# Kernel optimization log

Hardware: AMD Instinct MI355X
Metric: run time of the kernel (lower is better)

Reference implementation:

```python
import jax, jax.numpy as jnp
import numpy as np
import math

KERNEL_SIZES = [3, 5, 7, 7, 9, 9]
DILATIONS = [1, 2, 1, 3, 1, 2]
NUM_HEADS = 6
HEAD_DIM = 32  # in_channels 192 / 6 heads


def _neighborhood_patches(t, k, dil):
    """Equivalent of F.unfold(t, kernel_size=k, dilation=dil, padding=dil*(k//2)).
    t: [B, d, H, W] -> [B, d, k*k, H, W] (zero-padded borders, torch unfold ordering:
    patch index p = i*k + j over the kernel window, row-major)."""
    B, d, H, W = t.shape
    pad = dil * (k // 2)
    tp = jnp.pad(t, ((0, 0), (0, 0), (pad, pad), (pad, pad)))
    pats = [tp[:, :, i * dil:i * dil + H, j * dil:j * dil + W]
            for i in range(k) for j in range(k)]
    return jnp.stack(pats, axis=2)


def setup_inputs() -> dict:
    key = jax.random.key(0)
    ks = jax.random.split(key, 3 + NUM_HEADS)
    B, C, H, W = 4, 192, 96, 96
    x = jax.random.normal(ks[0], (B, C, H, W), dtype=jnp.float32)
    w_qkv = jax.random.normal(ks[1], (3 * C, C), dtype=jnp.float32) * 0.02  # 1x1 conv weight
    w_out = jax.random.normal(ks[2], (C, C), dtype=jnp.float32) * 0.02      # 1x1 conv weight
    inp = {"x": x, "w_qkv": w_qkv, "w_out": w_out}
    for i, k in enumerate(KERNEL_SIZES):
        # module inits biases to zeros; use small randn so softmax path is exercised
        inp[f"b{i}"] = jax.random.normal(ks[3 + i], (k * k,), dtype=jnp.float32) * 0.02
    return inp


def reference(x, w_qkv, w_out, b0, b1, b2, b3, b4, b5):
    biases = [b0, b1, b2, b3, b4, b5]
    B, C, H, W = x.shape
    scale = 1.0 / math.sqrt(HEAD_DIM)
    # 1x1 conv qkv projection
    qkv = jnp.einsum('bchw,oc->bohw', x, w_qkv)
    q, k, v = jnp.split(qkv, 3, axis=1)
    q = q.reshape(B, NUM_HEADS, HEAD_DIM, H, W)
    k = k.reshape(B, NUM_HEADS, HEAD_DIM, H, W)
    v = v.reshape(B, NUM_HEADS, HEAD_DIM, H, W)
    head_outs = []
    for i in range(NUM_HEADS):  # heads have structurally different (k, dilation)
        ksz, dil = KERNEL_SIZES[i], DILATIONS[i]
        kp = _neighborhood_patches(k[:, i], ksz, dil)  # [B, d, k*k, H, W]
        vp = _neighborhood_patches(v[:, i], ksz, dil)  # [B, d, k*k, H, W]
        scores = jnp.einsum('bdhw,bdphw->bphw', q[:, i], kp) * scale
        scores = scores + biases[i][None, :, None, None]
        attn = jax.nn.softmax(scores, axis=1)  # softmax over the k*k neighborhood
        head_outs.append(jnp.einsum('bphw,bdphw->bdhw', attn, vp))
    out = jnp.concatenate(head_outs, axis=1)  # [B, C, H, W]
    return jnp.einsum('bchw,oc->bohw', out, w_out)
```

## Files before the change

kernel.cpp:

```cpp
#include <hip/hip_runtime.h>
#include <hip/hip_bf16.h>
#include <math.h>

#define NPIX 9216
#define HDIM 96
#define WDIM 96
#define NHEADS 6
#define BATCH 4

typedef __bf16 bf16x8 __attribute__((ext_vector_type(8)));
typedef float  f32x4  __attribute__((ext_vector_type(4)));

struct Bias6 { const float* p[6]; };

__device__ __forceinline__ void cp16(void* ldst, const void* gsrc) {
    __builtin_amdgcn_global_load_lds(
        (const __attribute__((address_space(1))) unsigned int*)gsrc,
        (__attribute__((address_space(3))) unsigned int*)ldst, 16, 0, 0);
}

__device__ __forceinline__ unsigned short bfbits(__bf16 x) { return *(unsigned short*)&x; }

__device__ __forceinline__ unsigned packf16(float a, float b) {
    _Float16 ha = (_Float16)a, hb = (_Float16)b;
    return (unsigned)*(unsigned short*)&ha | ((unsigned)*(unsigned short*)&hb << 16);
}

template<int N>
__device__ __forceinline__ void waitcnt_vm() {
    if constexpr (N == 0) asm volatile("s_waitcnt vmcnt(0)" ::: "memory");
    else if constexpr (N == 2) asm volatile("s_waitcnt vmcnt(2)" ::: "memory");
    else if constexpr (N == 3) asm volatile("s_waitcnt vmcnt(3)" ::: "memory");
    else if constexpr (N == 5) asm volatile("s_waitcnt vmcnt(5)" ::: "memory");
    else asm volatile("s_waitcnt vmcnt(0)" ::: "memory");
    __builtin_amdgcn_sched_barrier(0);
}

#define MIX_LL(acc, kk, qq) asm("v_fma_mix_f32 %0, %1, %2, %0 op_sel:[0,0,0] op_sel_hi:[1,1,0]" : "+v"(acc) : "v"(kk), "v"(qq))
#define MIX_HH(acc, kk, qq) asm("v_fma_mix_f32 %0, %1, %2, %0 op_sel:[1,1,0] op_sel_hi:[1,1,0]" : "+v"(acc) : "v"(kk), "v"(qq))
#define MIX_LF(acc, vv, ee) asm("v_fma_mix_f32 %0, %1, %2, %0 op_sel:[0,0,0] op_sel_hi:[1,0,0]" : "+v"(acc) : "v"(vv), "v"(ee))
#define MIX_HF(acc, vv, ee) asm("v_fma_mix_f32 %0, %1, %2, %0 op_sel:[1,0,0] op_sel_hi:[1,0,0]" : "+v"(acc) : "v"(vv), "v"(ee))

__global__ __launch_bounds__(256) void convert_x(
    const float* __restrict__ x, __bf16* __restrict__ Xh,
    const float* __restrict__ w1, __bf16* __restrict__ h1, __bf16* __restrict__ l1,
    const float* __restrict__ w2, __bf16* __restrict__ h2, __bf16* __restrict__ l2)
{
    __shared__ float t[32][65];
    const int b  = blockIdx.z;
    const int c0 = blockIdx.y * 32;
    const int p0 = blockIdx.x * 64;
    const int tid = threadIdx.x;

    if (blockIdx.y == 0 && blockIdx.z == 0) {
        const int f = blockIdx.x * 256 + tid;
        #pragma unroll
        for (int u = 0; u < 4; ++u) {
            const int i = f * 4 + u;
            if (i < 576 * 192) {
                float v = w1[i]; __bf16 h = (__bf16)v;
                h1[i] = h; l1[i] = (__bf16)(v - (float)h);
            } else {
                const int j = i - 576 * 192;
                float v = w2[j]; __bf16 h = (__bf16)v;
                h2[j] = h; l2[j] = (__bf16)(v - (float)h);
            }
        }
    }

    const int pl = tid & 63;
    #pragma unroll
    for (int i = 0; i < 8; ++i) {
        const int c = i * 4 + (tid >> 6);
        t[c][pl] = x[((size_t)b * 192 + c0 + c) * NPIX + p0 + pl];
    }
    __syncthreads();
    const int p  = tid >> 2;
    const int cq = (tid & 3) * 8;
    bf16x8 vh;
    #pragma unroll
    for (int j = 0; j < 8; ++j)
        vh[j] = (__bf16)t[cq + j][p];
    *(bf16x8*)(Xh + ((size_t)b * NPIX + p0 + p) * 192 + c0 + cq) = vh;
}

template<int MODE, int TWO_FROM>
__global__ __launch_bounds__(256) void gemm_mfma(
    const __bf16* __restrict__ Ah, const __bf16* __restrict__ Al,
    const __bf16* __restrict__ Bh,
    void* __restrict__ Yv, int M)
{
    __shared__ __bf16 sAh[64 * 64];
    __shared__ __bf16 sAl[64 * 64];
    __shared__ __bf16 sBh[128 * 64];

    const int b  = blockIdx.z;
    const int n0 = blockIdx.x * 128;
    const int m0 = blockIdx.y * 64;
    const bool two = (TWO_FROM < 1024) && (m0 >= TWO_FROM);
    const int tid  = threadIdx.x;
    const int lane = tid & 63;
    const int wid  = tid >> 6;
    const int wr = wid >> 1, wc = wid & 1;
    const int lr = lane & 15;
    const int kg = lane >> 4;

    const char* gA_h = (const char*)Ah + (size_t)m0 * 384;
    const char* gA_l = (const char*)Al + (size_t)m0 * 384;
    const char* gB   = (const char*)Bh + ((size_t)b * NPIX + n0) * 384;

    f32x4 acc[2][4];
    #pragma unroll
    for (int mf = 0; mf < 2; ++mf)
        #pragma unroll
        for (int nf = 0; nf < 4; ++nf)
            acc[mf][nf] = (f32x4){0.f, 0.f, 0.f, 0.f};

    for (int ks = 0; ks < 3; ++ks) {
        if (ks) __syncthreads();
        const int kb = ks * 128;
        #pragma unroll
        for (int it = 0; it < 2; ++it) {
            const int d  = it * 256 + tid;
            const int rd = d >> 3, cd = d & 7;
            const size_t src = (size_t)rd * 384 + kb + ((cd ^ (rd & 7)) << 4);
            cp16((char*)sAh + d * 16, gA_h + src);
            if (two) cp16((char*)sAl + d * 16, gA_l + src);
        }
        #pragma unroll
        for (int it = 0; it < 4; ++it) {
            const int d  = it * 256 + tid;
            const int rd = d >> 3, cd = d & 7;
            const size_t src = (size_t)rd * 384 + kb + ((cd ^ (rd & 7)) << 4);
            cp16((char*)sBh + d * 16, gB + src);
        }
        __syncthreads();
        #pragma unroll
        for (int s = 0; s < 2; ++s) {
            bf16x8 aH[2], aL[2], bH[4];
            #pragma unroll
            for (int mf = 0; mf < 2; ++mf) {
                const int row = wr * 32 + mf * 16 + lr;
                const int c = (s * 4 + kg) ^ (row & 7);
                aH[mf] = *(const bf16x8*)((const char*)sAh + row * 128 + c * 16);
                if (two) aL[mf] = *(const bf16x8*)((const char*)sAl + row * 128 + c * 16);
            }
            #pragma unroll
            for (int nf = 0; nf < 4; ++nf) {
                const int row = wc * 64 + nf * 16 + lr;
                const int c = (s * 4 + kg) ^ (row & 7);
                bH[nf] = *(const bf16x8*)((const char*)sBh + row * 128 + c * 16);
            }
            #pragma unroll
            for (int mf = 0; mf < 2; ++mf)
                #pragma unroll
                for (int nf = 0; nf < 4; ++nf) {
                    acc[mf][nf] = __builtin_amdgcn_mfma_f32_16x16x32_bf16(aH[mf], bH[nf], acc[mf][nf], 0, 0, 0);
                    if (two)
                        acc[mf][nf] = __builtin_amdgcn_mfma_f32_16x16x32_bf16(aL[mf], bH[nf], acc[mf][nf], 0, 0, 0);
                }
        }
    }

    if (MODE == 0) {
        float* Yb = (float*)Yv + ((size_t)b * M + m0 + wr * 32) * NPIX + n0 + wc * 64;
        #pragma unroll
        for (int mf = 0; mf < 2; ++mf)
            #pragma unroll
            for (int r = 0; r < 4; ++r) {
                const int row = mf * 16 + kg * 4 + r;
                #pragma unroll
                for (int nf = 0; nf < 4; ++nf)
                    Yb[(size_t)row * NPIX + nf * 16 + lr] = acc[mf][nf][r];
            }
    } else {
        #pragma unroll
        for (int mf = 0; mf < 2; ++mf) {
            const int cbase = m0 + wr * 32 + mf * 16 + kg * 4;
            unsigned* Yq = (unsigned*)Yv
                + (((size_t)b * 72 + (cbase >> 3)) * NPIX + n0 + wc * 64 + lr) * 4
                + ((kg & 1) << 1);
            #pragma unroll
            for (int nf = 0; nf < 4; ++nf) {
                Yq[(nf * 16) * 4 + 0] = packf16(acc[mf][nf][0], acc[mf][nf][1]);
                Yq[(nf * 16) * 4 + 1] = packf16(acc[mf][nf][2], acc[mf][nf][3]);
            }
        }
    }
}

template<int KSZ, int DIL, bool DB, int L>
__device__ __forceinline__ void attn_body(
    const uint4* __restrict__ Qq, const uint4* __restrict__ Kq,
    const uint4* __restrict__ Vq, const float* __restrict__ bias,
    const uint4* __restrict__ guard,
    __bf16* __restrict__ oh, int h0, int w0,
    uint4* __restrict__ bufs,
    unsigned (* __restrict__ out_lds)[256])
{
    constexpr int CC  = KSZ / 2;
    constexpr int HAL = CC * DIL;
    constexpr int R   = 8 + 2 * HAL;
    constexpr int C   = 32 + 2 * HAL;
    constexpr int RC  = R * C;
    constexpr int NN  = KSZ * KSZ;

    const int tid = threadIdx.x;
    const int tx = tid & 31;
    const int ty = tid >> 5;
    const int pix = (h0 + ty) * WDIM + (w0 + tx);
    const int lb = ty * C + tx;

    uint4 qv[4];
    #pragma unroll
    for (int p = 0; p < 4; ++p) qv[p] = Qq[(size_t)p * NPIX + pix];

    float score[NN];
    #pragma unroll
    for (int n = 0; n < NN; ++n) score[n] = bias[n] * 5.656854249492381f;

    auto STAGE = [&](int r) {
        const uint4* src = (r < 4) ? (Kq + (size_t)r * NPIX)
                                   : (Vq + (size_t)(r - 4) * NPIX);
        uint4* dst = bufs + (DB ? ((r & 1) * (L * 256)) : 0);
        #pragma unroll
        for (int it = 0; it < L; ++it) {
            const int idx = it * 256 + tid;
            const int rr = idx / C, cc = idx - rr * C;
            const int gh = h0 - HAL + rr, gw = w0 - HAL + cc;
            const bool ok = (idx < RC) && ((unsigned)gh < (unsigned)HDIM)
                                       && ((unsigned)gw < (unsigned)WDIM);
            const uint4* s = ok ? (src + gh * WDIM + gw) : guard;
            cp16(dst + idx, s);
        }
    };

    auto QK = [&](const uint4* buf, int oct) {
        const uint4 q = qv[oct];
        #pragma unroll
        for (int i = 0; i < KSZ; ++i)
            #pragma unroll
            for (int j = 0; j < KSZ; ++j) {
                const uint4 k8 = buf[lb + i * DIL * C + j * DIL];
                float s = score[i * KSZ + j];
                MIX_LL(s, k8.x, q.x); MIX_HH(s, k8.x, q.x);
                MIX_LL(s, k8.y, q.y); MIX_HH(s, k8.y, q.y);
                MIX_LL(s, k8.z, q.z); MIX_HH(s, k8.z, q.z);
                MIX_LL(s, k8.w, q.w); MIX_HH(s, k8.w, q.w);
                score[i * KSZ + j] = s;
            }
    };

    float inv = 0.f;
    auto SOFTMAX = [&]() {
        float l = 0.f;
        #pragma unroll
        for (int n = 0; n < NN; ++n) {
            const float e = exp2f(score[n] * 0.25506113952980654f);
            l += e;
            score[n] = e;
        }
        inv = 1.f / l;
    };

    auto PV = [&](const uint4* buf, int oct) {
        float a0 = 0.f, a1 = 0.f, a2 = 0.f, a3 = 0.f;
        float a4 = 0.f, a5 = 0.f, a6 = 0.f, a7 = 0.f;
        #pragma unroll
        for (int i = 0; i < KSZ; ++i)
            #pragma unroll
            for (int j = 0; j < KSZ; ++j) {
                const uint4 v8 = buf[lb + i * DIL * C + j * DIL];
                const float e = score[i * KSZ + j];
                MIX_LF(a0, v8.x, e); MIX_HF(a1, v8.x, e);
                MIX_LF(a2, v8.y, e); MIX_HF(a3, v8.y, e);
                MIX_LF(a4, v8.z, e); MIX_HF(a5, v8.z, e);
                MIX_LF(a6, v8.w, e); MIX_HF(a7, v8.w, e);
            }
        const int rr = oct & 1;
        const __bf16 c0 = (__bf16)(a0 * inv), c1 = (__bf16)(a1 * inv);
        const __bf16 c2 = (__bf16)(a2 * inv), c3 = (__bf16)(a3 * inv);
        const __bf16 c4 = (__bf16)(a4 * inv), c5 = (__bf16)(a5 * inv);
        const __bf16 c6 = (__bf16)(a6 * inv), c7 = (__bf16)(a7 * inv);
        out_lds[rr * 4 + 0][tid] = (unsigned)bfbits(c0) | ((unsigned)bfbits(c1) << 16);
        out_lds[rr * 4 + 1][tid] = (unsigned)bfbits(c2) | ((unsigned)bfbits(c3) << 16);
        out_lds[rr * 4 + 2][tid] = (unsigned)bfbits(c4) | ((unsigned)bfbits(c5) << 16);
        out_lds[rr * 4 + 3][tid] = (unsigned)bfbits(c6) | ((unsigned)bfbits(c7) << 16);
    };

    auto COOP = [&](int half) {
        #pragma unroll
        for (int it = 0; it < 2; ++it) {
            const int linear = it * 256 + tid;
            const int px = linear >> 1;
            const int c  = linear & 1;
            const int gpix = (h0 + (px >> 5)) * WDIM + w0 + (px & 31);
            uint4 val = make_uint4(out_lds[c * 4 + 0][px], out_lds[c * 4 + 1][px],
                                   out_lds[c * 4 + 2][px], out_lds[c * 4 + 3][px]);
            *((uint4*)((unsigned*)(oh + (size_t)gpix * 192)) + half * 2 + c) = val;
        }
    };

    if constexpr (DB) {
        STAGE(0);
        #pragma unroll
        for (int r = 0; r < 8; ++r) {
            if (r < 7) STAGE(r + 1);
            if (r < 7) waitcnt_vm<L>(); else waitcnt_vm<0>();
            __builtin_amdgcn_s_barrier();
            __builtin_amdgcn_sched_barrier(0);
            const uint4* buf = bufs + (r & 1) * (L * 256);
            if (r < 4) {
                QK(buf, r);
                if (r == 3) SOFTMAX();
            } else {
                PV(buf, r - 4);
                asm volatile("s_waitcnt lgkmcnt(0)" ::: "memory");
                __builtin_amdgcn_sched_barrier(0);
            }
            __builtin_amdgcn_s_barrier();
            __builtin_amdgcn_sched_barrier(0);
            if (r == 5) COOP(0);
            if (r == 7) COOP(1);
        }
    } else {
        #pragma unroll
        for (int r = 0; r < 8; ++r) {
            __syncthreads();
            if (r == 6) COOP(0);
            STAGE(r);
            __syncthreads();
            const uint4* buf = bufs;
            if (r < 4) {
                QK(buf, r);
                if (r == 3) SOFTMAX();
            } else {
                PV(buf, r - 4);
            }
        }
        __syncthreads();
        COOP(1);
    }
}

__global__ __launch_bounds__(256) void attn_kernel(
    const uint4* __restrict__ qkv, Bias6 bs, __bf16* __restrict__ ATh,
    const uint4* __restrict__ guard)
{
    __shared__ uint4 bufs[2560];
    __shared__ unsigned out_lds[8][256];

    const int orig = blockIdx.x;
    const int wg = (orig & 7) * 108 + (orig >> 3);
    const int panel = wg / 36;
    const int tile = wg - panel * 36;
    const int chunk = panel / 3, slot = panel - chunk * 3;
    int head, b;
    if (slot == 0)      { head = 4 + (chunk >> 2); b = chunk & 3; }
    else if (slot == 1) { head = 2 + (chunk >> 2); b = chunk & 3; }
    else                { head = (chunk < 4) ? 1 : 0; b = chunk & 3; }
    const int tx = tile % 3, ty = tile / 3;
    const int w0 = tx * 32, h0 = ty * 8;

    const uint4* base = qkv + (size_t)b * 72 * NPIX;
    const uint4* Qq = base + (size_t)(head * 4) * NPIX;
    const uint4* Kq = base + (size_t)(24 + head * 4) * NPIX;
    const uint4* Vq = base + (size_t)(48 + head * 4) * NPIX;
    __bf16* oh = ATh + (size_t)b * NPIX * 192 + head * 32;
    const float* bias = bs.p[head];

    switch (head) {
        case 0: attn_body<3, 1, true, 2>(Qq, Kq, Vq, bias, guard, oh, h0, w0, bufs, out_lds); break;
        case 1: attn_body<5, 2, true, 3>(Qq, Kq, Vq, bias, guard, oh, h0, w0, bufs, out_lds); break;
        case 2: attn_body<7, 1, true, 3>(Qq, Kq, Vq, bias, guard, oh, h0, w0, bufs, out_lds); break;
        case 3: attn_body<7, 3, false, 6>(Qq, Kq, Vq, bias, guard, oh, h0, w0, bufs, out_lds); break;
        case 4: attn_body<9, 1, true, 3>(Qq, Kq, Vq, bias, guard, oh, h0, w0, bufs, out_lds); break;
        case 5: attn_body<9, 2, true, 5>(Qq, Kq, Vq, bias, guard, oh, h0, w0, bufs, out_lds); break;
    }
}

extern "C" void kernel_launch(void* const* d_in, const int* in_sizes, int n_in,
                              void* d_out, int out_size, void* d_ws, size_t ws_size,
                              hipStream_t stream) {
    const float* x     = (const float*)d_in[0];
    const float* w_qkv = (const float*)d_in[1];
    const float* w_out = (const float*)d_in[2];
    Bias6 bs;
    for (int i = 0; i < 6; ++i) bs.p[i] = (const float*)d_in[3 + i];
    float* out = (float*)d_out;

    char* ws = (char*)d_ws;
    uint4* QKV = (uint4*)ws;            ws += (size_t)BATCH * 72 * NPIX * 16;
    __bf16* Xh  = (__bf16*)ws;          ws += (size_t)BATCH * NPIX * 192 * 2;
    __bf16* ATh = (__bf16*)ws;          ws += (size_t)BATCH * NPIX * 192 * 2;
    __bf16* W1h = (__bf16*)ws;          ws += (size_t)576 * 192 * 2;
    __bf16* W1l = (__bf16*)ws;          ws += (size_t)576 * 192 * 2;
    __bf16* W2h = (__bf16*)ws;          ws += (size_t)192 * 192 * 2;
    __bf16* W2l = (__bf16*)ws;          ws += (size_t)192 * 192 * 2;
    uint4* guard = (uint4*)ws;          ws += 1024;

    hipMemsetAsync(guard, 0, 1024, stream);

    convert_x<<<dim3(NPIX / 64, 192 / 32, BATCH), 256, 0, stream>>>(
        x, Xh, w_qkv, W1h, W1l, w_out, W2h, W2l);

    gemm_mfma<1, 384><<<dim3(NPIX / 128, 576 / 64, BATCH), 256, 0, stream>>>(
        W1h, W1l, Xh, (void*)QKV, 576);

    attn_kernel<<<dim3(864), 256, 0, stream>>>(QKV, bs, ATh, guard);

    gemm_mfma<0, 1024><<<dim3(NPIX / 128, 192 / 64, BATCH), 256, 0, stream>>>(
        W2h, W2l, ATh, (void*)out, 192);
}
```

Baseline: 91.35 us.

## Switch GEMMs to fp16 single-pass MFMA and remap grid across XCDs

```diff
diff --git a/kernel.cpp b/kernel.cpp
--- a/kernel.cpp
+++ b/kernel.cpp
@@ -8,8 +8,8 @@
 #define NHEADS 6
 #define BATCH 4
 
-typedef __bf16 bf16x8 __attribute__((ext_vector_type(8)));
-typedef float  f32x4  __attribute__((ext_vector_type(4)));
+typedef _Float16 f16x8 __attribute__((ext_vector_type(8)));
+typedef float    f32x4 __attribute__((ext_vector_type(4)));
 
 struct Bias6 { const float* p[6]; };
 
@@ -18,8 +18,6 @@
         (const __attribute__((address_space(1))) unsigned int*)gsrc,
         (__attribute__((address_space(3))) unsigned int*)ldst, 16, 0, 0);
 }
-
-__device__ __forceinline__ unsigned short bfbits(__bf16 x) { return *(unsigned short*)&x; }
 
 __device__ __forceinline__ unsigned packf16(float a, float b) {
     _Float16 ha = (_Float16)a, hb = (_Float16)b;
@@ -42,9 +40,10 @@
 #define MIX_HF(acc, vv, ee) asm("v_fma_mix_f32 %0, %1, %2, %0 op_sel:[1,0,0] op_sel_hi:[1,0,0]" : "+v"(acc) : "v"(vv), "v"(ee))
 
 __global__ __launch_bounds__(256) void convert_x(
-    const float* __restrict__ x, __bf16* __restrict__ Xh,
-    const float* __restrict__ w1, __bf16* __restrict__ h1, __bf16* __restrict__ l1,
-    const float* __restrict__ w2, __bf16* __restrict__ h2, __bf16* __restrict__ l2)
+    const float* __restrict__ x, _Float16* __restrict__ Xf,
+    const float* __restrict__ w1, _Float16* __restrict__ Wf1,
+    const float* __restrict__ w2, _Float16* __restrict__ Wf2,
+    uint4* __restrict__ guard)
 {
     __shared__ float t[32][65];
     const int b  = blockIdx.z;
@@ -57,15 +56,11 @@
         #pragma unroll
         for (int u = 0; u < 4; ++u) {
             const int i = f * 4 + u;
-            if (i < 576 * 192) {
-                float v = w1[i]; __bf16 h = (__bf16)v;
-                h1[i] = h; l1[i] = (__bf16)(v - (float)h);
-            } else {
-                const int j = i - 576 * 192;
-                float v = w2[j]; __bf16 h = (__bf16)v;
-                h2[j] = h; l2[j] = (__bf16)(v - (float)h);
-            }
-        }
+            if (i < 576 * 192) Wf1[i] = (_Float16)w1[i];
+            else               Wf2[i - 576 * 192] = (_Float16)w2[i - 576 * 192];
+        }
+        if (blockIdx.x == 0 && tid < 64)
+            guard[tid] = make_uint4(0u, 0u, 0u, 0u);
     }
 
     const int pl = tid & 63;
@@ -77,27 +72,29 @@
     __syncthreads();
     const int p  = tid >> 2;
     const int cq = (tid & 3) * 8;
-    bf16x8 vh;
+    f16x8 vh;
     #pragma unroll
     for (int j = 0; j < 8; ++j)
-        vh[j] = (__bf16)t[cq + j][p];
-    *(bf16x8*)(Xh + ((size_t)b * NPIX + p0 + p) * 192 + c0 + cq) = vh;
-}
-
-template<int MODE, int TWO_FROM>
+        vh[j] = (_Float16)t[cq + j][p];
+    *(f16x8*)(Xf + ((size_t)b * NPIX + p0 + p) * 192 + c0 + cq) = vh;
+}
+
+template<int MODE, int M>
 __global__ __launch_bounds__(256) void gemm_mfma(
-    const __bf16* __restrict__ Ah, const __bf16* __restrict__ Al,
-    const __bf16* __restrict__ Bh,
-    void* __restrict__ Yv, int M)
+    const _Float16* __restrict__ A, const _Float16* __restrict__ B,
+    void* __restrict__ Yv)
 {
-    __shared__ __bf16 sAh[64 * 64];
-    __shared__ __bf16 sAl[64 * 64];
-    __shared__ __bf16 sBh[128 * 64];
-
-    const int b  = blockIdx.z;
-    const int n0 = blockIdx.x * 128;
-    const int m0 = blockIdx.y * 64;
-    const bool two = (TWO_FROM < 1024) && (m0 >= TWO_FROM);
+    constexpr int MT = M / 64;
+    __shared__ _Float16 sA[64 * 64];
+    __shared__ _Float16 sB[128 * 64];
+
+    const int orig = blockIdx.x;
+    const int xcd = orig & 7;
+    const int l = orig >> 3;
+    const int m0 = (l % MT) * 64;
+    const int b  = (l / MT) & 3;
+    const int n0 = (xcd * 9 + l / (MT * 4)) * 128;
+
     const int tid  = threadIdx.x;
     const int lane = tid & 63;
     const int wid  = tid >> 6;
@@ -105,9 +102,8 @@
     const int lr = lane & 15;
     const int kg = lane >> 4;
 
-    const char* gA_h = (const char*)Ah + (size_t)m0 * 384;
-    const char* gA_l = (const char*)Al + (size_t)m0 * 384;
-    const char* gB   = (const char*)Bh + ((size_t)b * NPIX + n0) * 384;
+    const char* gA = (const char*)A + (size_t)m0 * 384;
+    const char* gB = (const char*)B + ((size_t)b * NPIX + n0) * 384;
 
     f32x4 acc[2][4];
     #pragma unroll
@@ -124,41 +120,36 @@
             const int d  = it * 256 + tid;
             const int rd = d >> 3, cd = d & 7;
             const size_t src = (size_t)rd * 384 + kb + ((cd ^ (rd & 7)) << 4);
-            cp16((char*)sAh + d * 16, gA_h + src);
-            if (two) cp16((char*)sAl + d * 16, gA_l + src);
+            cp16((char*)sA + d * 16, gA + src);
         }
         #pragma unroll
         for (int it = 0; it < 4; ++it) {
             const int d  = it * 256 + tid;
             const int rd = d >> 3, cd = d & 7;
             const size_t src = (size_t)rd * 384 + kb + ((cd ^ (rd & 7)) << 4);
-            cp16((char*)sBh + d * 16, gB + src);
+            cp16((char*)sB + d * 16, gB + src);
         }
         __syncthreads();
         #pragma unroll
         for (int s = 0; s < 2; ++s) {
-            bf16x8 aH[2], aL[2], bH[4];
+            f16x8 aH[2], bH[4];
             #pragma unroll
             for (int mf = 0; mf < 2; ++mf) {
                 const int row = wr * 32 + mf * 16 + lr;
                 const int c = (s * 4 + kg) ^ (row & 7);
-                aH[mf] = *(const bf16x8*)((const char*)sAh + row * 128 + c * 16);
-                if (two) aL[mf] = *(const bf16x8*)((const char*)sAl + row * 128 + c * 16);
+                aH[mf] = *(const f16x8*)((const char*)sA + row * 128 + c * 16);
             }
             #pragma unroll
             for (int nf = 0; nf < 4; ++nf) {
                 const int row = wc * 64 + nf * 16 + lr;
                 const int c = (s * 4 + kg) ^ (row & 7);
-                bH[nf] = *(const bf16x8*)((const char*)sBh + row * 128 + c * 16);
+                bH[nf] = *(const f16x8*)((const char*)sB + row * 128 + c * 16);
             }
             #pragma unroll
             for (int mf = 0; mf < 2; ++mf)
                 #pragma unroll
-                for (int nf = 0; nf < 4; ++nf) {
-                    acc[mf][nf] = __builtin_amdgcn_mfma_f32_16x16x32_bf16(aH[mf], bH[nf], acc[mf][nf], 0, 0, 0);
-                    if (two)
-                        acc[mf][nf] = __builtin_amdgcn_mfma_f32_16x16x32_bf16(aL[mf], bH[nf], acc[mf][nf], 0, 0, 0);
-                }
+                for (int nf = 0; nf < 4; ++nf)
+                    acc[mf][nf] = __builtin_amdgcn_mfma_f32_16x16x32_f16(aH[mf], bH[nf], acc[mf][nf], 0, 0, 0);
         }
     }
 
@@ -194,7 +185,7 @@
     const uint4* __restrict__ Qq, const uint4* __restrict__ Kq,
     const uint4* __restrict__ Vq, const float* __restrict__ bias,
     const uint4* __restrict__ guard,
-    __bf16* __restrict__ oh, int h0, int w0,
+    _Float16* __restrict__ oh, int h0, int w0,
     uint4* __restrict__ bufs,
     unsigned (* __restrict__ out_lds)[256])
 {
@@ -278,14 +269,10 @@
                 MIX_LF(a6, v8.w, e); MIX_HF(a7, v8.w, e);
             }
         const int rr = oct & 1;
-        const __bf16 c0 = (__bf16)(a0 * inv), c1 = (__bf16)(a1 * inv);
-        const __bf16 c2 = (__bf16)(a2 * inv), c3 = (__bf16)(a3 * inv);
-        const __bf16 c4 = (__bf16)(a4 * inv), c5 = (__bf16)(a5 * inv);
-        const __bf16 c6 = (__bf16)(a6 * inv), c7 = (__bf16)(a7 * inv);
-        out_lds[rr * 4 + 0][tid] = (unsigned)bfbits(c0) | ((unsigned)bfbits(c1) << 16);
-        out_lds[rr * 4 + 1][tid] = (unsigned)bfbits(c2) | ((unsigned)bfbits(c3) << 16);
-        out_lds[rr * 4 + 2][tid] = (unsigned)bfbits(c4) | ((unsigned)bfbits(c5) << 16);
-        out_lds[rr * 4 + 3][tid] = (unsigned)bfbits(c6) | ((unsigned)bfbits(c7) << 16);
+        out_lds[rr * 4 + 0][tid] = packf16(a0 * inv, a1 * inv);
+        out_lds[rr * 4 + 1][tid] = packf16(a2 * inv, a3 * inv);
+        out_lds[rr * 4 + 2][tid] = packf16(a4 * inv, a5 * inv);
+        out_lds[rr * 4 + 3][tid] = packf16(a6 * inv, a7 * inv);
     };
 
     auto COOP = [&](int half) {
@@ -344,10 +331,10 @@
 }
 
 __global__ __launch_bounds__(256) void attn_kernel(
-    const uint4* __restrict__ qkv, Bias6 bs, __bf16* __restrict__ ATh,
+    const uint4* __restrict__ qkv, Bias6 bs, _Float16* __restrict__ ATf,
     const uint4* __restrict__ guard)
 {
-    __shared__ uint4 bufs[2560];
+    __shared__ uint4 bufs[1536];
     __shared__ unsigned out_lds[8][256];
 
     const int orig = blockIdx.x;
@@ -366,7 +353,7 @@
     const uint4* Qq = base + (size_t)(head * 4) * NPIX;
     const uint4* Kq = base + (size_t)(24 + head * 4) * NPIX;
     const uint4* Vq = base + (size_t)(48 + head * 4) * NPIX;
-    __bf16* oh = ATh + (size_t)b * NPIX * 192 + head * 32;
+    _Float16* oh = ATf + (size_t)b * NPIX * 192 + head * 32;
     const float* bias = bs.p[head];
 
     switch (head) {
@@ -375,7 +362,7 @@
         case 2: attn_body<7, 1, true, 3>(Qq, Kq, Vq, bias, guard, oh, h0, w0, bufs, out_lds); break;
         case 3: attn_body<7, 3, false, 6>(Qq, Kq, Vq, bias, guard, oh, h0, w0, bufs, out_lds); break;
         case 4: attn_body<9, 1, true, 3>(Qq, Kq, Vq, bias, guard, oh, h0, w0, bufs, out_lds); break;
-        case 5: attn_body<9, 2, true, 5>(Qq, Kq, Vq, bias, guard, oh, h0, w0, bufs, out_lds); break;
+        case 5: attn_body<9, 2, false, 5>(Qq, Kq, Vq, bias, guard, oh, h0, w0, bufs, out_lds); break;
     }
 }
 
@@ -390,25 +377,21 @@
     float* out = (float*)d_out;
 
     char* ws = (char*)d_ws;
-    uint4* QKV = (uint4*)ws;            ws += (size_t)BATCH * 72 * NPIX * 16;
-    __bf16* Xh  = (__bf16*)ws;          ws += (size_t)BATCH * NPIX * 192 * 2;
-    __bf16* ATh = (__bf16*)ws;          ws += (size_t)BATCH * NPIX * 192 * 2;
-    __bf16* W1h = (__bf16*)ws;          ws += (size_t)576 * 192 * 2;
-    __bf16* W1l = (__bf16*)ws;          ws += (size_t)576 * 192 * 2;
-    __bf16* W2h = (__bf16*)ws;          ws += (size_t)192 * 192 * 2;
-    __bf16* W2l = (__bf16*)ws;          ws += (size_t)192 * 192 * 2;
-    uint4* guard = (uint4*)ws;          ws += 1024;
-
-    hipMemsetAsync(guard, 0, 1024, stream);
+    uint4*    QKV = (uint4*)ws;         ws += (size_t)BATCH * 72 * NPIX * 16;
+    _Float16* Xf  = (_Float16*)ws;      ws += (size_t)BATCH * NPIX * 192 * 2;
+    _Float16* ATf = (_Float16*)ws;      ws += (size_t)BATCH * NPIX * 192 * 2;
+    _Float16* Wf1 = (_Float16*)ws;      ws += (size_t)576 * 192 * 2;
+    _Float16* Wf2 = (_Float16*)ws;      ws += (size_t)192 * 192 * 2;
+    uint4* guard  = (uint4*)ws;         ws += 1024;
 
     convert_x<<<dim3(NPIX / 64, 192 / 32, BATCH), 256, 0, stream>>>(
-        x, Xh, w_qkv, W1h, W1l, w_out, W2h, W2l);
-
-    gemm_mfma<1, 384><<<dim3(NPIX / 128, 576 / 64, BATCH), 256, 0, stream>>>(
-        W1h, W1l, Xh, (void*)QKV, 576);
-
-    attn_kernel<<<dim3(864), 256, 0, stream>>>(QKV, bs, ATh, guard);
-
-    gemm_mfma<0, 1024><<<dim3(NPIX / 128, 192 / 64, BATCH), 256, 0, stream>>>(
-        W2h, W2l, ATh, (void*)out, 192);
-}
+        x, Xf, w_qkv, Wf1, w_out, Wf2, guard);
+
+    gemm_mfma<1, 576><<<dim3(8 * (576 / 64) * 4 * 9), 256, 0, stream>>>(
+        Wf1, Xf, (void*)QKV);
+
+    attn_kernel<<<dim3(864), 256, 0, stream>>>(QKV, bs, ATf, guard);
+
+    gemm_mfma<0, 192><<<dim3(8 * (192 / 64) * 4 * 9), 256, 0, stream>>>(
+        Wf2, ATf, (void*)out);
+}
```

Measured after the change: 83.89 us. -8.2%, faster.
